# Optimization experiments

Hardware: AMD Instinct MI355X
Metric: run time of the kernel (lower is better)

## Reference

```python
import jax, jax.numpy as jnp
import numpy as np
from jax import lax

B, N, C = 8, 1024, 768
H, D = 12, 64
K = 3  # conv kernel size


def dwconv_over_batch(x, w, b):
    """Faithful port of SpatialDepthWisePerHeadConvolution as used in this module.
    x: [B, N, H, D]. The original code treats dim0 (B) as the conv length axis.
    w: [H*D, 1, K] depthwise kernel, b: [H*D].
    Returns [B, N, H, D].
    """
    b_, n_, h_, d_ = x.shape
    xc = jnp.transpose(x, (1, 2, 3, 0)).reshape(n_, h_ * d_, b_)  # [N, HD, B]
    y = lax.conv_general_dilated(
        xc, w, window_strides=(1,), padding=[(K - 1, K - 1)],
        feature_group_count=h_ * d_, dimension_numbers=("NCH", "OIH", "NCH"))
    y = y[:, :, :b_] + b[None, :, None]  # causal slice (drop last K-1)
    return jnp.transpose(y.reshape(n_, h_, d_, b_), (3, 0, 1, 2))


def setup_inputs() -> dict:
    key = jax.random.key(0)
    ks = jax.random.split(key, 12)
    s = 0.02
    inp = {
        "x": jax.random.normal(ks[0], (B, N, C), jnp.float32),
        "wq": jax.random.normal(ks[1], (C, H * D), jnp.float32) * s,
        "wk": jax.random.normal(ks[2], (C, H * D), jnp.float32) * s,
        "wv": jax.random.normal(ks[3], (C, H * D), jnp.float32) * s,
        "bv": jnp.zeros((H * D,), jnp.float32),
        "cq_w": jax.random.normal(ks[4], (H * D, 1, K), jnp.float32) * s,
        "cq_b": jnp.zeros((H * D,), jnp.float32),
        "ck_w": jax.random.normal(ks[5], (H * D, 1, K), jnp.float32) * s,
        "ck_b": jnp.zeros((H * D,), jnp.float32),
        "cv_w": jax.random.normal(ks[6], (H * D, 1, K), jnp.float32) * s,
        "cv_b": jnp.zeros((H * D,), jnp.float32),
        "wo": jax.random.normal(ks[7], (C, C), jnp.float32) * s,
        "bo": jnp.zeros((C,), jnp.float32),
    }
    return inp


def reference(x, wq, wk, wv, bv, cq_w, cq_b, ck_w, ck_b, cv_w, cv_b, wo, bo):
    scale = (C // H) ** -0.5
    # linear -> [B,N,H,D]
    q = (x @ wq).reshape(B, N, H, D)
    k = (x @ wk).reshape(B, N, H, D)
    v = ((x @ wv) + bv).reshape(B, N, H, D)
    # per-head depthwise causal conv (over batch axis, as in the original code)
    q = dwconv_over_batch(q, cq_w, cq_b)
    k = dwconv_over_batch(k, ck_w, ck_b)
    v = dwconv_over_batch(v, cv_w, cv_b)
    # [B,H,N,D]
    q = jnp.transpose(q, (0, 2, 1, 3))
    k = jnp.transpose(k, (0, 2, 1, 3))
    v = jnp.transpose(v, (0, 2, 1, 3))
    scores = jnp.einsum("bhnd,bhmd->bhnm", q, k) * scale
    attn = jax.nn.softmax(scores, axis=-1)
    out = jnp.einsum("bhnm,bhmd->bhnd", attn, v)
    out = jnp.transpose(out, (0, 2, 1, 3)).reshape(B, N, C)
    return out @ wo + bo
```

## Files before the change

kernel.cpp:

```cpp
#include <hip/hip_runtime.h>
#include <math.h>

static constexpr int B_ = 8, N_ = 1024, C_ = 768, H_ = 12, D_ = 64;

typedef __bf16 bf16_t;
typedef bf16_t bf16x8 __attribute__((ext_vector_type(8)));
typedef float f32x4 __attribute__((ext_vector_type(4)));

#define MFMA16(a, b, c) __builtin_amdgcn_mfma_f32_16x16x32_bf16((a), (b), (c), 0, 0, 0)

__device__ __forceinline__ unsigned short f2bf(float f) {
    unsigned u = __builtin_bit_cast(unsigned, f);
    u += 0x7FFFu + ((u >> 16) & 1u);
    return (unsigned short)(u >> 16);
}

__device__ __forceinline__ void gload16(void* lds, const void* g) {
    __builtin_amdgcn_global_load_lds(
        (const __attribute__((address_space(1))) unsigned int*)g,
        (__attribute__((address_space(3))) unsigned int*)lds, 16, 0, 0);
}

__device__ __forceinline__ int swz(int row, int kslot) {
    return row * 128 + (((kslot ^ row) & 7) << 4);
}

__global__ __launch_bounds__(256)
void castx_kernel(const float* __restrict__ in, unsigned short* __restrict__ out)
{
    const int i = blockIdx.x * 256 + threadIdx.x;
    const float4 a = ((const float4*)in)[2 * i];
    const float4 b = ((const float4*)in)[2 * i + 1];
    uint4 o;
    o.x = f2bf(a.x) | ((unsigned)f2bf(a.y) << 16);
    o.y = f2bf(a.z) | ((unsigned)f2bf(a.w) << 16);
    o.z = f2bf(b.x) | ((unsigned)f2bf(b.y) << 16);
    o.w = f2bf(b.z) | ((unsigned)f2bf(b.w) << 16);
    ((uint4*)out)[i] = o;
}

__global__ __launch_bounds__(256)
void castwT_kernel(const float* __restrict__ w, unsigned short* __restrict__ wT)
{
    __shared__ float T[64][65];
    const int t = threadIdx.x;
    const int k0 = blockIdx.x * 64, n0 = blockIdx.y * 64;
    const int r = t >> 2, c0 = (t & 3) * 16;
#pragma unroll
    for (int j4 = 0; j4 < 4; ++j4) {
        const float4 v = *(const float4*)(w + (size_t)(k0 + r) * 768 + n0 + c0 + j4 * 4);
        T[r][c0 + j4 * 4 + 0] = v.x; T[r][c0 + j4 * 4 + 1] = v.y;
        T[r][c0 + j4 * 4 + 2] = v.z; T[r][c0 + j4 * 4 + 3] = v.w;
    }
    __syncthreads();
    const int nn = t >> 2;
    unsigned short o[16];
#pragma unroll
    for (int j = 0; j < 16; ++j) o[j] = f2bf(T[c0 + j][nn]);
    uint4* dst = (uint4*)(wT + (size_t)(n0 + nn) * 768 + k0 + c0);
    dst[0] = *(uint4*)(o); dst[1] = *(uint4*)(o + 8);
}

__global__ __launch_bounds__(256)
void gemm_bf16(const unsigned short* __restrict__ A, const unsigned short* __restrict__ BT,
               const float* __restrict__ bias, float* __restrict__ Cmat,
               int M, int Ncols, int Kdim)
{
    __shared__ char As[128 * 128];
    __shared__ char Bs[128 * 128];

    const int tid = threadIdx.x, lane = tid & 63, w = tid >> 6;
    const int wr = w >> 1, wc = w & 1;
    const int slot = lane & 7, rsub = lane >> 3;
    const int row0 = blockIdx.x * 128, col0 = blockIdx.y * 128;

    f32x4 acc[4][4] = {};

    for (int k0 = 0; k0 < Kdim; k0 += 64) {
#pragma unroll
        for (int c = 0; c < 4; ++c) {
            const int chunk = c * 4 + w;
            const int r = chunk * 8 + rsub;
            gload16(As + chunk * 1024, A + (size_t)(row0 + r) * Kdim + k0 + 8 * (slot ^ (r & 7)));
            gload16(Bs + chunk * 1024, BT + (size_t)(col0 + r) * Kdim + k0 + 8 * (slot ^ (r & 7)));
        }
        __syncthreads();

#pragma unroll
        for (int kk = 0; kk < 2; ++kk) {
            const int kslot = kk * 4 + (lane >> 4);
            bf16x8 af[4], bf[4];
#pragma unroll
            for (int mi = 0; mi < 4; ++mi)
                af[mi] = *(const bf16x8*)(As + swz(wr * 64 + mi * 16 + (lane & 15), kslot));
#pragma unroll
            for (int ni = 0; ni < 4; ++ni)
                bf[ni] = *(const bf16x8*)(Bs + swz(wc * 64 + ni * 16 + (lane & 15), kslot));
#pragma unroll
            for (int mi = 0; mi < 4; ++mi)
#pragma unroll
                for (int ni = 0; ni < 4; ++ni)
                    acc[mi][ni] = MFMA16(af[mi], bf[ni], acc[mi][ni]);
        }
        __syncthreads();
    }

#pragma unroll
    for (int mi = 0; mi < 4; ++mi) {
        const int row = row0 + wr * 64 + mi * 16 + ((lane >> 4) << 2);
#pragma unroll
        for (int ni = 0; ni < 4; ++ni) {
            const int col = col0 + wc * 64 + ni * 16 + (lane & 15);
            const float bv_ = bias ? bias[col] : 0.f;
#pragma unroll
            for (int r = 0; r < 4; ++r)
                Cmat[(size_t)(row + r) * Ncols + col] = acc[mi][ni][r] + bv_;
        }
    }
}

__global__ __launch_bounds__(256)
void dwconv_bf16(const float* __restrict__ lin, const float* __restrict__ w,
                 const float* __restrict__ bias, unsigned short* __restrict__ out)
{
    const int i = blockIdx.x * 256 + threadIdx.x;
    const int c4 = i % (C_ / 4);
    const int n  = (i / (C_ / 4)) % N_;
    const int b  = i / ((C_ / 4) * N_);
    const int c  = c4 * 4;

    float4 x0 = make_float4(0.f, 0.f, 0.f, 0.f);
    float4 x1 = x0;
    if (b >= 2) x0 = *(const float4*)(lin + ((size_t)(b - 2) * N_ + n) * C_ + c);
    if (b >= 1) x1 = *(const float4*)(lin + ((size_t)(b - 1) * N_ + n) * C_ + c);
    const float4 x2 = *(const float4*)(lin + ((size_t)b * N_ + n) * C_ + c);
    const float4 bb = *(const float4*)(bias + c);

    float4 y;
    y.x = fmaf(w[(c + 0) * 3 + 0], x0.x, fmaf(w[(c + 0) * 3 + 1], x1.x, fmaf(w[(c + 0) * 3 + 2], x2.x, bb.x)));
    y.y = fmaf(w[(c + 1) * 3 + 0], x0.y, fmaf(w[(c + 1) * 3 + 1], x1.y, fmaf(w[(c + 1) * 3 + 2], x2.y, bb.y)));
    y.z = fmaf(w[(c + 2) * 3 + 0], x0.z, fmaf(w[(c + 2) * 3 + 1], x1.z, fmaf(w[(c + 2) * 3 + 2], x2.z, bb.z)));
    y.w = fmaf(w[(c + 3) * 3 + 0], x0.w, fmaf(w[(c + 3) * 3 + 1], x1.w, fmaf(w[(c + 3) * 3 + 2], x2.w, bb.w)));

    const int h = c / D_, d = c % D_;
    ushort4 o;
    o.x = f2bf(y.x); o.y = f2bf(y.y); o.z = f2bf(y.z); o.w = f2bf(y.w);
    *(ushort4*)(out + (((size_t)b * H_ + h) * N_ + n) * D_ + d) = o;
}

__global__ __launch_bounds__(256)
void transpose64(const unsigned short* __restrict__ in, unsigned short* __restrict__ out)
{
    __shared__ unsigned short T[64][67];
    const int t = threadIdx.x;
    const int bh = blockIdx.y, n0 = blockIdx.x * 64;
    const int r = t >> 2, c0 = (t & 3) * 16;

    const uint4* src = (const uint4*)(in + ((size_t)bh * N_ + n0 + r) * 64 + c0);
    unsigned short tmp[16];
    *(uint4*)(tmp) = src[0];
    *(uint4*)(tmp + 8) = src[1];
#pragma unroll
    for (int j = 0; j < 16; ++j) T[r][c0 + j] = tmp[j];
    __syncthreads();

    const int d = t >> 2;
    unsigned short o[16];
#pragma unroll
    for (int j = 0; j < 16; ++j) o[j] = T[c0 + j][d];
    uint4* dst = (uint4*)(out + ((size_t)bh * 64 + d) * N_ + n0 + c0);
    dst[0] = *(uint4*)(o); dst[1] = *(uint4*)(o + 8);
}

__global__ __launch_bounds__(256)
void attn_mfma(const unsigned short* __restrict__ Qg, const unsigned short* __restrict__ Kg,
               const unsigned short* __restrict__ Vtg, unsigned short* __restrict__ Og)
{
    __shared__ char Pb[16384];
    __shared__ char Kb[2][8192];
    __shared__ char Vb[2][8192];

    const int tid = threadIdx.x, lane = tid & 63, w = tid >> 6;
    const int slot = lane & 7, rsub = lane >> 3;
    const int bh = blockIdx.y, b = bh / H_, h = bh % H_;
    const int q0 = blockIdx.x * 128;

    const unsigned short* Qp = Qg + (size_t)bh * N_ * 64;
    const unsigned short* Kp = Kg + (size_t)bh * N_ * 64;
    const unsigned short* Vp = Vtg + (size_t)bh * 64 * N_;

#pragma unroll
    for (int c = 0; c < 4; ++c) {
        const int chunk = c * 4 + w;
        const int r = chunk * 8 + rsub;
        gload16(Pb + chunk * 1024, Qp + (size_t)(q0 + r) * 64 + 8 * (slot ^ (r & 7)));
    }
#pragma unroll
    for (int c = 0; c < 2; ++c) {
        const int chunk = c * 4 + w;
        const int r = chunk * 8 + rsub;
        gload16(Kb[0] + chunk * 1024, Kp + (size_t)r * 64 + 8 * (slot ^ (r & 7)));
        gload16(Vb[0] + chunk * 1024, Vp + (size_t)r * N_ + 8 * (slot ^ (r & 7)));
    }
    __syncthreads();

    bf16x8 qf[2][2];
#pragma unroll
    for (int mi = 0; mi < 2; ++mi)
#pragma unroll
        for (int kk = 0; kk < 2; ++kk)
            qf[mi][kk] = *(const bf16x8*)(Pb + swz(w * 32 + mi * 16 + (lane & 15), kk * 4 + (lane >> 4)));

    f32x4 o[2][4] = {};
    float mrow[2][4], lrow[2][4];
#pragma unroll
    for (int mi = 0; mi < 2; ++mi)
#pragma unroll
        for (int r = 0; r < 4; ++r) { mrow[mi][r] = -1e30f; lrow[mi][r] = 0.f; }

    int buf = 0;
    for (int kt = 0; kt < N_ / 64; ++kt) {
        if (kt < N_ / 64 - 1) {
            const int nb = buf ^ 1;
#pragma unroll
            for (int c = 0; c < 2; ++c) {
                const int chunk = c * 4 + w;
                const int r = chunk * 8 + rsub;
                gload16(Kb[nb] + chunk * 1024, Kp + (size_t)((kt + 1) * 64 + r) * 64 + 8 * (slot ^ (r & 7)));
                gload16(Vb[nb] + chunk * 1024, Vp + (size_t)r * N_ + (kt + 1) * 64 + 8 * (slot ^ (r & 7)));
            }
        }

        f32x4 s[2][4] = {};
#pragma unroll
        for (int kk = 0; kk < 2; ++kk) {
            const int kslot = kk * 4 + (lane >> 4);
            bf16x8 kf[4];
#pragma unroll
            for (int ni = 0; ni < 4; ++ni)
                kf[ni] = *(const bf16x8*)(Kb[buf] + swz(ni * 16 + (lane & 15), kslot));
#pragma unroll
            for (int mi = 0; mi < 2; ++mi)
#pragma unroll
                for (int ni = 0; ni < 4; ++ni)
                    s[mi][ni] = MFMA16(qf[mi][kk], kf[ni], s[mi][ni]);
        }

#pragma unroll
        for (int mi = 0; mi < 2; ++mi) {
            float pv[4][4];
#pragma unroll
            for (int r = 0; r < 4; ++r) {
                const float a0 = s[mi][0][r] * 0.125f, a1 = s[mi][1][r] * 0.125f;
                const float a2 = s[mi][2][r] * 0.125f, a3 = s[mi][3][r] * 0.125f;
                pv[r][0] = a0; pv[r][1] = a1; pv[r][2] = a2; pv[r][3] = a3;
                float m0 = fmaxf(fmaxf(a0, a1), fmaxf(a2, a3));
#pragma unroll
                for (int mk = 1; mk < 16; mk <<= 1) m0 = fmaxf(m0, __shfl_xor(m0, mk));
                const float mold = mrow[mi][r];
                const float mnew = fmaxf(mold, m0);
                const float f = __expf(mold - mnew);
                mrow[mi][r] = mnew;
                float ssum = 0.f;
#pragma unroll
                for (int ni = 0; ni < 4; ++ni) {
                    const float e = __expf(pv[r][ni] - mnew);
                    pv[r][ni] = e; ssum += e;
                }
#pragma unroll
                for (int mk = 1; mk < 16; mk <<= 1) ssum += __shfl_xor(ssum, mk);
                lrow[mi][r] = lrow[mi][r] * f + ssum;
#pragma unroll
                for (int nd = 0; nd < 4; ++nd) o[mi][nd][r] *= f;
            }
            const int prow_base = w * 32 + mi * 16 + ((lane >> 4) << 2);
#pragma unroll
            for (int r = 0; r < 4; ++r) {
                const int m = prow_base + r;
                const int rowoff = m * 128, sw = (m & 7) << 4;
#pragma unroll
                for (int ni = 0; ni < 4; ++ni) {
                    const int col = ni * 16 + (lane & 15);
                    *(unsigned short*)(Pb + rowoff + ((col * 2) ^ sw)) = f2bf(pv[r][ni]);
                }
            }
        }

#pragma unroll
        for (int kk = 0; kk < 2; ++kk) {
            const int kslot = kk * 4 + (lane >> 4);
            bf16x8 pa[2], vf[4];
#pragma unroll
            for (int mi = 0; mi < 2; ++mi)
                pa[mi] = *(const bf16x8*)(Pb + swz(w * 32 + mi * 16 + (lane & 15), kslot));
#pragma unroll
            for (int nd = 0; nd < 4; ++nd)
                vf[nd] = *(const bf16x8*)(Vb[buf] + swz(nd * 16 + (lane & 15), kslot));
#pragma unroll
            for (int mi = 0; mi < 2; ++mi)
#pragma unroll
                for (int nd = 0; nd < 4; ++nd)
                    o[mi][nd] = MFMA16(pa[mi], vf[nd], o[mi][nd]);
        }

        __syncthreads();
        buf ^= 1;
    }

#pragma unroll
    for (int mi = 0; mi < 2; ++mi)
#pragma unroll
        for (int r = 0; r < 4; ++r) {
            const float inv = 1.0f / lrow[mi][r];
            const int qrow = q0 + w * 32 + mi * 16 + ((lane >> 4) << 2) + r;
            unsigned short* orow = Og + ((size_t)b * N_ + qrow) * C_ + h * D_ + (lane & 15);
#pragma unroll
            for (int nd = 0; nd < 4; ++nd) orow[nd * 16] = f2bf(o[mi][nd][r] * inv);
        }
}

extern "C" void kernel_launch(void* const* d_in, const int* in_sizes, int n_in,
                              void* d_out, int out_size, void* d_ws, size_t ws_size,
                              hipStream_t stream)
{
    (void)in_sizes; (void)n_in; (void)out_size; (void)ws_size;
    const float* x    = (const float*)d_in[0];
    const float* wq   = (const float*)d_in[1];
    const float* wk   = (const float*)d_in[2];
    const float* wv   = (const float*)d_in[3];
    const float* bv   = (const float*)d_in[4];
    const float* cq_w = (const float*)d_in[5];
    const float* cq_b = (const float*)d_in[6];
    const float* ck_w = (const float*)d_in[7];
    const float* ck_b = (const float*)d_in[8];
    const float* cv_w = (const float*)d_in[9];
    const float* cv_b = (const float*)d_in[10];
    const float* wo   = (const float*)d_in[11];
    const float* bo   = (const float*)d_in[12];
    float* out = (float*)d_out;

    char* wsb = (char*)d_ws;
    const size_t T = (size_t)B_ * N_ * C_;
    const size_t WB = 2 * 589824;
    unsigned short* xb  = (unsigned short*)wsb;
    unsigned short* wqT = (unsigned short*)(wsb + 2 * T);
    unsigned short* wkT = wqT + 589824;
    unsigned short* wvT = wkT + 589824;
    float* q_lin = (float*)(wsb + 2 * T + 3 * WB);
    float* k_lin = q_lin + T;
    float* v_lin = k_lin + T;
    unsigned short* qc = (unsigned short*)(v_lin + T);
    unsigned short* kc = qc + T;
    unsigned short* vtmp = xb;
    unsigned short* vt   = (unsigned short*)q_lin;
    unsigned short* attn_out = (unsigned short*)k_lin;
    unsigned short* woT = (unsigned short*)((char*)k_lin + 2 * T);

    const int M = B_ * N_;

    castx_kernel<<<dim3((int)(T / 8 / 256)), 256, 0, stream>>>(x, xb);
    castwT_kernel<<<dim3(12, 12), 256, 0, stream>>>(wq, wqT);
    castwT_kernel<<<dim3(12, 12), 256, 0, stream>>>(wk, wkT);
    castwT_kernel<<<dim3(12, 12), 256, 0, stream>>>(wv, wvT);

    gemm_bf16<<<dim3(M / 128, C_ / 128), 256, 0, stream>>>(xb, wqT, nullptr, q_lin, M, C_, C_);
    gemm_bf16<<<dim3(M / 128, C_ / 128), 256, 0, stream>>>(xb, wkT, nullptr, k_lin, M, C_, C_);
    gemm_bf16<<<dim3(M / 128, C_ / 128), 256, 0, stream>>>(xb, wvT, bv,      v_lin, M, C_, C_);

    const int convBlocks = (B_ * N_ * (C_ / 4)) / 256;
    dwconv_bf16<<<convBlocks, 256, 0, stream>>>(q_lin, cq_w, cq_b, qc);
    dwconv_bf16<<<convBlocks, 256, 0, stream>>>(k_lin, ck_w, ck_b, kc);
    dwconv_bf16<<<convBlocks, 256, 0, stream>>>(v_lin, cv_w, cv_b, vtmp);

    transpose64<<<dim3(N_ / 64, B_ * H_), 256, 0, stream>>>(vtmp, vt);
    castwT_kernel<<<dim3(12, 12), 256, 0, stream>>>(wo, woT);

    attn_mfma<<<dim3(N_ / 128, B_ * H_), 256, 0, stream>>>(qc, kc, vt, attn_out);

    gemm_bf16<<<dim3(M / 128, C_ / 128), 256, 0, stream>>>(attn_out, woT, bo, out, M, C_, C_);
}
```

Baseline: 320.0 us.

## Batch QKV GEMMs, store bf16 intermediates, fuse V conv with transpose

After: 308.3 us. 3.7% less time.

```diff
diff --git a/kernel.cpp b/kernel.cpp
--- a/kernel.cpp
+++ b/kernel.cpp
@@ -7,12 +7,16 @@
 typedef bf16_t bf16x8 __attribute__((ext_vector_type(8)));
 typedef float f32x4 __attribute__((ext_vector_type(4)));
 
-#define MFMA16(a, b, c) __builtin_amdgcn_mfma_f32_16x16x32_bf16((a), (b), (c), 0, 0, 0)
+#define MFMA32(a, b, c) __builtin_amdgcn_mfma_f32_16x16x32_bf16((a), (b), (c), 0, 0, 0)
 
 __device__ __forceinline__ unsigned short f2bf(float f) {
     unsigned u = __builtin_bit_cast(unsigned, f);
     u += 0x7FFFu + ((u >> 16) & 1u);
     return (unsigned short)(u >> 16);
+}
+
+__device__ __forceinline__ float bf2f(unsigned short u) {
+    return __builtin_bit_cast(float, (unsigned)u << 16);
 }
 
 __device__ __forceinline__ void gload16(void* lds, const void* g) {
@@ -40,8 +44,17 @@
 }
 
 __global__ __launch_bounds__(256)
-void castwT_kernel(const float* __restrict__ w, unsigned short* __restrict__ wT)
-{
+void castwT4_kernel(const float* w0, const float* w1, const float* w2, const float* w3,
+                    unsigned short* o0, unsigned short* o1,
+                    unsigned short* o2, unsigned short* o3)
+{
+    const float* w; unsigned short* wT;
+    switch (blockIdx.z) {
+        case 0:  w = w0; wT = o0; break;
+        case 1:  w = w1; wT = o1; break;
+        case 2:  w = w2; wT = o2; break;
+        default: w = w3; wT = o3; break;
+    }
     __shared__ float T[64][65];
     const int t = threadIdx.x;
     const int k0 = blockIdx.x * 64, n0 = blockIdx.y * 64;
@@ -61,10 +74,12 @@
     dst[0] = *(uint4*)(o); dst[1] = *(uint4*)(o + 8);
 }
 
-__global__ __launch_bounds__(256)
-void gemm_bf16(const unsigned short* __restrict__ A, const unsigned short* __restrict__ BT,
-               const float* __restrict__ bias, float* __restrict__ Cmat,
-               int M, int Ncols, int Kdim)
+template <typename OutT>
+__device__ __forceinline__ void gemm_body(const unsigned short* __restrict__ A,
+                                          const unsigned short* __restrict__ BT,
+                                          const float* __restrict__ bias,
+                                          OutT* __restrict__ Cmat,
+                                          int Ncols, int Kdim, int row0, int col0)
 {
     __shared__ char As[128 * 128];
     __shared__ char Bs[128 * 128];
@@ -72,7 +87,6 @@
     const int tid = threadIdx.x, lane = tid & 63, w = tid >> 6;
     const int wr = w >> 1, wc = w & 1;
     const int slot = lane & 7, rsub = lane >> 3;
-    const int row0 = blockIdx.x * 128, col0 = blockIdx.y * 128;
 
     f32x4 acc[4][4] = {};
 
@@ -100,7 +114,7 @@
             for (int mi = 0; mi < 4; ++mi)
 #pragma unroll
                 for (int ni = 0; ni < 4; ++ni)
-                    acc[mi][ni] = MFMA16(af[mi], bf[ni], acc[mi][ni]);
+                    acc[mi][ni] = MFMA32(af[mi], bf[ni], acc[mi][ni]);
         }
         __syncthreads();
     }
@@ -113,63 +127,117 @@
             const int col = col0 + wc * 64 + ni * 16 + (lane & 15);
             const float bv_ = bias ? bias[col] : 0.f;
 #pragma unroll
-            for (int r = 0; r < 4; ++r)
-                Cmat[(size_t)(row + r) * Ncols + col] = acc[mi][ni][r] + bv_;
-        }
-    }
-}
-
-__global__ __launch_bounds__(256)
-void dwconv_bf16(const float* __restrict__ lin, const float* __restrict__ w,
-                 const float* __restrict__ bias, unsigned short* __restrict__ out)
-{
+            for (int r = 0; r < 4; ++r) {
+                const float v = acc[mi][ni][r] + bv_;
+                if constexpr (sizeof(OutT) == 2)
+                    Cmat[(size_t)(row + r) * Ncols + col] = (OutT)f2bf(v);
+                else
+                    Cmat[(size_t)(row + r) * Ncols + col] = v;
+            }
+        }
+    }
+}
+
+__global__ __launch_bounds__(256)
+void gemm_qkv(const unsigned short* __restrict__ xb,
+              const unsigned short* __restrict__ wqT, const unsigned short* __restrict__ wkT,
+              const unsigned short* __restrict__ wvT, const float* __restrict__ bv,
+              unsigned short* __restrict__ q_lin, unsigned short* __restrict__ k_lin,
+              unsigned short* __restrict__ v_lin)
+{
+    const int by = blockIdx.y, sel = by / 6, colt = by % 6;
+    const unsigned short* BT; unsigned short* dst; const float* bias = nullptr;
+    if (sel == 0)      { BT = wqT; dst = q_lin; }
+    else if (sel == 1) { BT = wkT; dst = k_lin; }
+    else               { BT = wvT; dst = v_lin; bias = bv; }
+    gemm_body<unsigned short>(xb, BT, bias, dst, C_, C_, blockIdx.x * 128, colt * 128);
+}
+
+__global__ __launch_bounds__(256)
+void gemm_proj(const unsigned short* __restrict__ A, const unsigned short* __restrict__ BT,
+               const float* __restrict__ bias, float* __restrict__ Cmat)
+{
+    gemm_body<float>(A, BT, bias, Cmat, C_, C_, blockIdx.x * 128, blockIdx.y * 128);
+}
+
+__global__ __launch_bounds__(256)
+void dwconv_qk(const unsigned short* __restrict__ qlin, const unsigned short* __restrict__ klin,
+               const float* __restrict__ cq_w, const float* __restrict__ cq_b,
+               const float* __restrict__ ck_w, const float* __restrict__ ck_b,
+               unsigned short* __restrict__ qc, unsigned short* __restrict__ kc)
+{
+    const unsigned short* lin; const float* w; const float* bias;
+    unsigned short* out;
+    if (blockIdx.y == 0) { lin = qlin; w = cq_w; bias = cq_b; out = qc; }
+    else                 { lin = klin; w = ck_w; bias = ck_b; out = kc; }
+
     const int i = blockIdx.x * 256 + threadIdx.x;
-    const int c4 = i % (C_ / 4);
-    const int n  = (i / (C_ / 4)) % N_;
-    const int b  = i / ((C_ / 4) * N_);
-    const int c  = c4 * 4;
-
-    float4 x0 = make_float4(0.f, 0.f, 0.f, 0.f);
-    float4 x1 = x0;
-    if (b >= 2) x0 = *(const float4*)(lin + ((size_t)(b - 2) * N_ + n) * C_ + c);
-    if (b >= 1) x1 = *(const float4*)(lin + ((size_t)(b - 1) * N_ + n) * C_ + c);
-    const float4 x2 = *(const float4*)(lin + ((size_t)b * N_ + n) * C_ + c);
-    const float4 bb = *(const float4*)(bias + c);
-
-    float4 y;
-    y.x = fmaf(w[(c + 0) * 3 + 0], x0.x, fmaf(w[(c + 0) * 3 + 1], x1.x, fmaf(w[(c + 0) * 3 + 2], x2.x, bb.x)));
-    y.y = fmaf(w[(c + 1) * 3 + 0], x0.y, fmaf(w[(c + 1) * 3 + 1], x1.y, fmaf(w[(c + 1) * 3 + 2], x2.y, bb.y)));
-    y.z = fmaf(w[(c + 2) * 3 + 0], x0.z, fmaf(w[(c + 2) * 3 + 1], x1.z, fmaf(w[(c + 2) * 3 + 2], x2.z, bb.z)));
-    y.w = fmaf(w[(c + 3) * 3 + 0], x0.w, fmaf(w[(c + 3) * 3 + 1], x1.w, fmaf(w[(c + 3) * 3 + 2], x2.w, bb.w)));
-
-    const int h = c / D_, d = c % D_;
-    ushort4 o;
-    o.x = f2bf(y.x); o.y = f2bf(y.y); o.z = f2bf(y.z); o.w = f2bf(y.w);
-    *(ushort4*)(out + (((size_t)b * H_ + h) * N_ + n) * D_ + d) = o;
-}
-
-__global__ __launch_bounds__(256)
-void transpose64(const unsigned short* __restrict__ in, unsigned short* __restrict__ out)
-{
-    __shared__ unsigned short T[64][67];
+    const int c8 = i % (C_ / 8);
+    const int n  = (i / (C_ / 8)) % N_;
+    const int b  = i / ((C_ / 8) * N_);
+    const int c  = c8 * 8;
+
+    const uint4 z4 = make_uint4(0, 0, 0, 0);
+    const uint4 x0 = (b >= 2) ? *(const uint4*)(lin + ((size_t)(b - 2) * N_ + n) * C_ + c) : z4;
+    const uint4 x1 = (b >= 1) ? *(const uint4*)(lin + ((size_t)(b - 1) * N_ + n) * C_ + c) : z4;
+    const uint4 x2 = *(const uint4*)(lin + ((size_t)b * N_ + n) * C_ + c);
+    const unsigned short* u0 = (const unsigned short*)&x0;
+    const unsigned short* u1 = (const unsigned short*)&x1;
+    const unsigned short* u2 = (const unsigned short*)&x2;
+
+    unsigned short y[8];
+#pragma unroll
+    for (int j = 0; j < 8; ++j) {
+        const float v = w[(c + j) * 3 + 0] * bf2f(u0[j]) +
+                        w[(c + j) * 3 + 1] * bf2f(u1[j]) +
+                        w[(c + j) * 3 + 2] * bf2f(u2[j]) + bias[c + j];
+        y[j] = f2bf(v);
+    }
+    const int h = c8 >> 3, d0 = (c8 & 7) * 8;
+    *(uint4*)(out + (((size_t)b * H_ + h) * N_ + n) * 64 + d0) = *(uint4*)y;
+}
+
+__global__ __launch_bounds__(256)
+void conv_v_transpose(const unsigned short* __restrict__ vlin, const float* __restrict__ w,
+                      const float* __restrict__ bias, unsigned short* __restrict__ vt)
+{
+    __shared__ unsigned short T[64][72];
     const int t = threadIdx.x;
-    const int bh = blockIdx.y, n0 = blockIdx.x * 64;
+    const int n0 = blockIdx.x * 64, bh = blockIdx.y;
+    const int b = bh / H_, h = bh % H_;
     const int r = t >> 2, c0 = (t & 3) * 16;
-
-    const uint4* src = (const uint4*)(in + ((size_t)bh * N_ + n0 + r) * 64 + c0);
+    const int cbase = h * 64 + c0;
+
+    float acc[16];
+#pragma unroll
+    for (int i = 0; i < 16; ++i) acc[i] = bias[cbase + i];
+#pragma unroll
+    for (int j = 0; j < 3; ++j) {
+        const int bb = b - 2 + j;
+        if (bb < 0) continue;
+        const unsigned short* src = vlin + ((size_t)bb * N_ + n0 + r) * C_ + cbase;
+        const uint4 va = *(const uint4*)src;
+        const uint4 vb2 = *(const uint4*)(src + 8);
+        const unsigned short* u = (const unsigned short*)&va;
+        const unsigned short* u2 = (const unsigned short*)&vb2;
+#pragma unroll
+        for (int i = 0; i < 8; ++i)  acc[i]     += w[(cbase + i) * 3 + j] * bf2f(u[i]);
+#pragma unroll
+        for (int i = 0; i < 8; ++i)  acc[8 + i] += w[(cbase + 8 + i) * 3 + j] * bf2f(u2[i]);
+    }
     unsigned short tmp[16];
-    *(uint4*)(tmp) = src[0];
-    *(uint4*)(tmp + 8) = src[1];
-#pragma unroll
-    for (int j = 0; j < 16; ++j) T[r][c0 + j] = tmp[j];
+#pragma unroll
+    for (int i = 0; i < 16; ++i) tmp[i] = f2bf(acc[i]);
+    *(uint4*)&T[r][c0] = *(uint4*)tmp;
+    *(uint4*)&T[r][c0 + 8] = *(uint4*)(tmp + 8);
     __syncthreads();
 
     const int d = t >> 2;
     unsigned short o[16];
 #pragma unroll
-    for (int j = 0; j < 16; ++j) o[j] = T[c0 + j][d];
-    uint4* dst = (uint4*)(out + ((size_t)bh * 64 + d) * N_ + n0 + c0);
-    dst[0] = *(uint4*)(o); dst[1] = *(uint4*)(o + 8);
+    for (int i = 0; i < 16; ++i) o[i] = T[c0 + i][d];
+    uint4* dst = (uint4*)(vt + ((size_t)bh * 64 + d) * N_ + n0 + c0);
+    dst[0] = *(uint4*)o; dst[1] = *(uint4*)(o + 8);
 }
 
 __global__ __launch_bounds__(256)
@@ -182,8 +250,11 @@
 
     const int tid = threadIdx.x, lane = tid & 63, w = tid >> 6;
     const int slot = lane & 7, rsub = lane >> 3;
-    const int bh = blockIdx.y, b = bh / H_, h = bh % H_;
-    const int q0 = blockIdx.x * 128;
+
+    const int id = blockIdx.x;
+    const int bh = (id & 7) * 12 + ((id >> 3) % 12);
+    const int q0 = (id / 96) * 128;
+    const int b = bh / H_, h = bh % H_;
 
     const unsigned short* Qp = Qg + (size_t)bh * N_ * 64;
     const unsigned short* Kp = Kg + (size_t)bh * N_ * 64;
@@ -243,7 +314,7 @@
             for (int mi = 0; mi < 2; ++mi)
 #pragma unroll
                 for (int ni = 0; ni < 4; ++ni)
-                    s[mi][ni] = MFMA16(qf[mi][kk], kf[ni], s[mi][ni]);
+                    s[mi][ni] = MFMA32(qf[mi][kk], kf[ni], s[mi][ni]);
         }
 
 #pragma unroll
@@ -300,7 +371,7 @@
             for (int mi = 0; mi < 2; ++mi)
 #pragma unroll
                 for (int nd = 0; nd < 4; ++nd)
-                    o[mi][nd] = MFMA16(pa[mi], vf[nd], o[mi][nd]);
+                    o[mi][nd] = MFMA32(pa[mi], vf[nd], o[mi][nd]);
         }
 
         __syncthreads();
@@ -340,42 +411,34 @@
     float* out = (float*)d_out;
 
     char* wsb = (char*)d_ws;
-    const size_t T = (size_t)B_ * N_ * C_;
-    const size_t WB = 2 * 589824;
+    const size_t T  = (size_t)B_ * N_ * C_;
+    const size_t WB = (size_t)2 * 589824;
     unsigned short* xb  = (unsigned short*)wsb;
     unsigned short* wqT = (unsigned short*)(wsb + 2 * T);
     unsigned short* wkT = wqT + 589824;
     unsigned short* wvT = wkT + 589824;
-    float* q_lin = (float*)(wsb + 2 * T + 3 * WB);
-    float* k_lin = q_lin + T;
-    float* v_lin = k_lin + T;
-    unsigned short* qc = (unsigned short*)(v_lin + T);
-    unsigned short* kc = qc + T;
-    unsigned short* vtmp = xb;
-    unsigned short* vt   = (unsigned short*)q_lin;
-    unsigned short* attn_out = (unsigned short*)k_lin;
-    unsigned short* woT = (unsigned short*)((char*)k_lin + 2 * T);
+    unsigned short* woT = wvT + 589824;
+    char* p = wsb + 2 * T + 4 * WB;
+    unsigned short* q_lin = (unsigned short*)p;          p += 2 * T;
+    unsigned short* k_lin = (unsigned short*)p;          p += 2 * T;
+    unsigned short* v_lin = (unsigned short*)p;          p += 2 * T;
+    unsigned short* qc    = (unsigned short*)p;          p += 2 * T;
+    unsigned short* kc    = (unsigned short*)p;          p += 2 * T;
+    unsigned short* vt    = (unsigned short*)p;          p += 2 * T;
+    unsigned short* attn_out = xb;
 
     const int M = B_ * N_;
 
     castx_kernel<<<dim3((int)(T / 8 / 256)), 256, 0, stream>>>(x, xb);
-    castwT_kernel<<<dim3(12, 12), 256, 0, stream>>>(wq, wqT);
-    castwT_kernel<<<dim3(12, 12), 256, 0, stream>>>(wk, wkT);
-    castwT_kernel<<<dim3(12, 12), 256, 0, stream>>>(wv, wvT);
-
-    gemm_bf16<<<dim3(M / 128, C_ / 128), 256, 0, stream>>>(xb, wqT, nullptr, q_lin, M, C_, C_);
-    gemm_bf16<<<dim3(M / 128, C_ / 128), 256, 0, stream>>>(xb, wkT, nullptr, k_lin, M, C_, C_);
-    gemm_bf16<<<dim3(M / 128, C_ / 128), 256, 0, stream>>>(xb, wvT, bv,      v_lin, M, C_, C_);
-
-    const int convBlocks = (B_ * N_ * (C_ / 4)) / 256;
-    dwconv_bf16<<<convBlocks, 256, 0, stream>>>(q_lin, cq_w, cq_b, qc);
-    dwconv_bf16<<<convBlocks, 256, 0, stream>>>(k_lin, ck_w, ck_b, kc);
-    dwconv_bf16<<<convBlocks, 256, 0, stream>>>(v_lin, cv_w, cv_b, vtmp);
-
-    transpose64<<<dim3(N_ / 64, B_ * H_), 256, 0, stream>>>(vtmp, vt);
-    castwT_kernel<<<dim3(12, 12), 256, 0, stream>>>(wo, woT);
-
-    attn_mfma<<<dim3(N_ / 128, B_ * H_), 256, 0, stream>>>(qc, kc, vt, attn_out);
-
-    gemm_bf16<<<dim3(M / 128, C_ / 128), 256, 0, stream>>>(attn_out, woT, bo, out, M, C_, C_);
-}
+    castwT4_kernel<<<dim3(12, 12, 4), 256, 0, stream>>>(wq, wk, wv, wo, wqT, wkT, wvT, woT);
+
+    gemm_qkv<<<dim3(M / 128, 18), 256, 0, stream>>>(xb, wqT, wkT, wvT, bv, q_lin, k_lin, v_lin);
+
+    dwconv_qk<<<dim3((int)(T / 8 / 256), 2), 256, 0, stream>>>(
+        q_lin, k_lin, cq_w, cq_b, ck_w, ck_b, qc, kc);
+    conv_v_transpose<<<dim3(N_ / 64, B_ * H_), 256, 0, stream>>>(v_lin, cv_w, cv_b, vt);
+
+    attn_mfma<<<dim3(768), 256, 0, stream>>>(qc, kc, vt, attn_out);
+
+    gemm_proj<<<dim3(M / 128, C_ / 128), 256, 0, stream>>>(attn_out, woT, bo, out);
+}
```
